# Kernel optimization log

Measured on AMD Instinct MI355X. Metric: run time of the kernel, lower is better.

Reference implementation:

```python
import jax, jax.numpy as jnp
import numpy as np

# dims: batch, samples, agents, obs_dim, action_dim, hidden
B, S, N, D, A, H = 512, 64, 8, 64, 16, 256
IN_DIM = (D + A) * N  # 640


def mish(x):
    return x * jnp.tanh(jax.nn.softplus(x))


def setup_inputs() -> dict:
    key = jax.random.key(0)
    ks = jax.random.split(key, 9)
    u = lambda k, shape, fan_in: jax.random.uniform(
        k, shape, jnp.float32, -1.0 / np.sqrt(fan_in), 1.0 / np.sqrt(fan_in))
    return {
        "state": jax.random.normal(ks[0], (B, N, D), jnp.float32),
        "action": jax.random.normal(ks[1], (B, N, A), jnp.float32),
        "W1": u(ks[2], (IN_DIM, H), IN_DIM),
        "b1": u(ks[3], (H,), IN_DIM),
        "W2": u(ks[4], (H, H), H),
        "b2": u(ks[5], (H,), H),
        "W3": u(ks[6], (H, 1), H),
        "b3": u(ks[7], (1,), H),
        # random grand-coalition permutations of the N agents, per (batch, sample)
        "perm": jnp.argsort(jax.random.uniform(ks[8], (B, S, N)), axis=-1).astype(jnp.int32),
    }


def reference(state, action, W1, b1, W2, b2, W3, b3, perm):
    # subcoalition mask [B,S,N,N]: torch builds one-hot(perm) @ tril(ones),
    # i.e. mask[b,s,i,j] = 1 iff j <= perm[b,s,i]
    subcoal = (jnp.arange(N) <= perm[..., None]).astype(state.dtype)
    # gathered actions in coalition order [B,S,N,A]: act_g[b,s,j] = action[b, perm[b,s,j]]
    act_g = action[jnp.arange(B)[:, None, None], perm]
    # masked subcoalition actions [B,S,N,N,A] -> [B,S,N,N*A]
    act = (act_g[:, :, None, :, :] * subcoal[..., None]).reshape(B, S, N, N * A)
    # flattened global obs broadcast over (sample, agent) axes [B,S,N,N*D]
    obs = jnp.broadcast_to(state.reshape(B, 1, 1, N * D), (B, S, N, N * D))
    x = jnp.concatenate([obs, act], axis=-1)  # [B,S,N,IN_DIM]
    # per-agent loop in torch uses shared q1 weights -> single batched MLP
    h = mish(x @ W1 + b1)
    h = mish(h @ W2 + b2)
    q = h @ W3 + b3                   # [B,S,N,1]
    q1 = q.mean(axis=1).squeeze(-1)   # mean over samples -> [B,N]
    return (q1, q1)
```

## Files before the change

### kernel.cpp

```cpp
#include <hip/hip_runtime.h>

typedef unsigned short ushort_t;
typedef _Float16 half_t;
typedef __attribute__((ext_vector_type(2))) _Float16 half2_t;
typedef __attribute__((ext_vector_type(8))) _Float16 half8_t;
typedef __attribute__((ext_vector_type(2))) __fp16 fp16x2;
typedef __attribute__((ext_vector_type(2))) float fx2;
typedef __attribute__((ext_vector_type(4))) float floatx4;

#define LOG2E 1.4426950408889634f
#define LN2   0.6931471805599453f

__device__ __forceinline__ float exp2_(float x) {
#if __has_builtin(__builtin_amdgcn_exp2f)
    return __builtin_amdgcn_exp2f(x);
#else
    return exp2f(x);
#endif
}

__device__ __forceinline__ half2_t cvt_pk_f16(float a, float b) {
    auto r = __builtin_amdgcn_cvt_pkrtz(a, b);
    return __builtin_bit_cast(half2_t, r);
}

__device__ __forceinline__ float fdot2_(half2_t a, half2_t b) {
#if __has_builtin(__builtin_amdgcn_fdot2)
    return __builtin_amdgcn_fdot2(__builtin_bit_cast(fp16x2, a),
                                  __builtin_bit_cast(fp16x2, b), 0.0f, false);
#else
    return (float)a.x * (float)b.x + (float)a.y * (float)b.y;
#endif
}

__device__ __forceinline__ fx2 mish2(fx2 t0) {
    fx2 one = {1.0f, 1.0f};
    fx2 m2  = {-2.0f, -2.0f};
    fx2 u   = {exp2_(t0.x), exp2_(t0.y)};
    fx2 s   = u + one;
    fx2 wv  = __builtin_elementwise_fma(s, s, one);
    fx2 rr  = {__builtin_amdgcn_rcpf(wv.x), __builtin_amdgcn_rcpf(wv.y)};
    fx2 v   = __builtin_elementwise_fma(rr, m2, one);
    return t0 * v;
}

__device__ __forceinline__ float dpp_sum16(float v) {
    int x = __float_as_int(v);
    v += __int_as_float(__builtin_amdgcn_update_dpp(0, x, 0xB1, 0xF, 0xF, true));
    x = __float_as_int(v);
    v += __int_as_float(__builtin_amdgcn_update_dpp(0, x, 0x4E, 0xF, 0xF, true));
    x = __float_as_int(v);
    v += __int_as_float(__builtin_amdgcn_update_dpp(0, x, 0x124, 0xF, 0xF, true));
    x = __float_as_int(v);
    v += __int_as_float(__builtin_amdgcn_update_dpp(0, x, 0x128, 0xF, 0xF, true));
    return v;
}

__global__ __launch_bounds__(256) void prep_kernel(
        const float* __restrict__ state,
        const float* __restrict__ action,
        const float* __restrict__ W1,
        const float* __restrict__ W2,
        float* __restrict__ obsWp,
        half_t* __restrict__ actW,
        half_t* __restrict__ W2T,
        float* __restrict__ out) {
    int bid = blockIdx.x;
    int t = threadIdx.x;
    if (bid < 512) {
        int bg = bid >> 3;
        int kc = bid & 7;
        int bs = bg * 8;
        const float* w1p = W1 + (size_t)(kc * 64) * 256 + t;
        const float* stp = state + (size_t)bs * 512 + kc * 64;
        float acc[8];
#pragma unroll
        for (int bb = 0; bb < 8; ++bb) acc[bb] = 0.f;
#pragma unroll 4
        for (int f = 0; f < 64; ++f) {
            float w = w1p[f * 256];
#pragma unroll
            for (int bb = 0; bb < 8; ++bb)
                acc[bb] = fmaf(stp[bb * 512 + f], w, acc[bb]);
        }
#pragma unroll
        for (int bb = 0; bb < 8; ++bb)
            obsWp[(size_t)kc * 131072 + (bs + bb) * 256 + t] = acc[bb];
    } else if (bid < 1536) {
        int idx = bid - 512;
        int j = idx & 7;
        int b0 = (idx >> 3) * 4;
        const float* W1a = W1 + (size_t)(512 + j * 16) * 256;
        float wv[16];
#pragma unroll
        for (int a = 0; a < 16; ++a) wv[a] = W1a[a * 256 + t];
#pragma unroll
        for (int bb = 0; bb < 4; ++bb) {
            int b = b0 + bb;
            const float* acp = action + (size_t)b * 128;
            float acc[8];
#pragma unroll
            for (int n = 0; n < 8; ++n) acc[n] = 0.f;
#pragma unroll
            for (int a = 0; a < 16; ++a) {
#pragma unroll
                for (int n = 0; n < 8; ++n)
                    acc[n] = fmaf(acp[n * 16 + a], wv[a], acc[n]);
            }
#pragma unroll
            for (int n = 0; n < 8; ++n)
                actW[(((size_t)b * 8 + n) * 8 + j) * 256 + t] = (half_t)(acc[n] * LOG2E);
        }
    } else {
        int blk = bid - 1536;
        if (blk < 16) {
            out[blk * 512 + t] = 0.0f;
            out[blk * 512 + 256 + t] = 0.0f;
        }
        int n = blk * 8 + (t >> 5);
        int klo = t & 31;
#pragma unroll
        for (int kk = 0; kk < 8; ++kk) {
            int k = kk * 32 + klo;
            W2T[n * 256 + k] = (half_t)W2[k * 256 + n];
        }
    }
}

#define CHUNK_US 528

__global__ __launch_bounds__(512, 4) void main_kernel(
        const float* __restrict__ obsWp, const half_t* __restrict__ actW,
        const half_t* __restrict__ W2T, const int* __restrict__ perm,
        const float* __restrict__ b1, const float* __restrict__ b2,
        const float* __restrict__ W3, const float* __restrict__ b3,
        float* __restrict__ out) {
    __shared__ __align__(16) ushort_t h1[2][32 * CHUNK_US];
    __shared__ __align__(16) float obsb[256];
    __shared__ int perm_s[128];
    __shared__ float qpart[2][8][64];

    int t = threadIdx.x;
    int bid = blockIdx.x;
    int b = (bid & 7) * 64 + ((bid >> 3) & 63);
    int sgp = bid >> 9;
    int s0 = sgp * 16;

    int w = t >> 6;
    int L = t & 63;
    int lo = L & 15;
    int q = L >> 4;

    const half_t* w2base = W2T + ((size_t)(w * 32 + lo)) * 256 + q * 8;
    half8_t bpre[4];
    bpre[0] = *reinterpret_cast<const half8_t*>(w2base + 0 * 4096 + 0 * 32);
    bpre[1] = *reinterpret_cast<const half8_t*>(w2base + 1 * 4096 + 0 * 32);
    bpre[2] = *reinterpret_cast<const half8_t*>(w2base + 0 * 4096 + 1 * 32);
    bpre[3] = *reinterpret_cast<const half8_t*>(w2base + 1 * 4096 + 1 * 32);

    int col0 = w * 32 + lo;
    int col1 = col0 + 16;
    fx2 b2p = {b2[col0] * LOG2E, b2[col1] * LOG2E};
    half2_t w3p = cvt_pk_f16(W3[col0] * LN2, W3[col1] * LN2);

    const int* prow = perm + ((size_t)b * 64 + s0 + w) * 8;
    int4 pa0 = *reinterpret_cast<const int4*>(prow);
    int4 pa1 = *reinterpret_cast<const int4*>(prow + 4);
    int4 pb0 = *reinterpret_cast<const int4*>(prow + 64);
    int4 pb1 = *reinterpret_cast<const int4*>(prow + 68);

    if (t < 256) {
        float s = b1[t];
#pragma unroll
        for (int c = 0; c < 8; ++c) s += obsWp[(size_t)c * 131072 + b * 256 + t];
        obsb[t] = s * LOG2E;
    } else if (t < 384) {
        perm_s[t - 256] = perm[((size_t)b * 64 + s0) * 8 + (t - 256)];
    }

    int g = L >> 1;
    int ksg = g >> 2;
    int qq = g & 3;
    int halfsel = L & 1;
    const half_t* actg = actW + (size_t)b * 64 * 256 + L * 4;
    int dstoff = qq * 128 + halfsel * 4 + ksg * CHUNK_US;

    int pj0[8] = {pa0.x, pa0.y, pa0.z, pa0.w, pa1.x, pa1.y, pa1.z, pa1.w};
    uint2 av0[8];
#pragma unroll
    for (int j = 0; j < 8; ++j)
        av0[j] = *reinterpret_cast<const uint2*>(actg + (pj0[j] * 8 + j) * 256);

    __syncthreads();

    float4 ob = *reinterpret_cast<const float4*>(obsb + L * 4);

    {
        fx2 r01 = {ob.x, ob.y};
        fx2 r23 = {ob.z, ob.w};
        ushort_t* dst0 = h1[0] + dstoff;
#pragma unroll
        for (int j = 0; j < 8; ++j) {
            half2_t a0 = __builtin_bit_cast(half2_t, av0[j].x);
            half2_t a1 = __builtin_bit_cast(half2_t, av0[j].y);
            r01 += (fx2){(float)a0.x, (float)a0.y};
            r23 += (fx2){(float)a1.x, (float)a1.y};
            fx2 h01 = mish2(r01);
            fx2 h23 = mish2(r23);
            int row = w * 8 + j;
            int mt2 = row >> 4, lr = row & 15;
            uint2 pk = make_uint2(__builtin_bit_cast(unsigned, cvt_pk_f16(h01.x, h01.y)),
                                  __builtin_bit_cast(unsigned, cvt_pk_f16(h23.x, h23.y)));
            *reinterpret_cast<uint2*>(dst0 + mt2 * 8 * CHUNK_US + lr * 8) = pk;
        }
    }

    int pj1[8] = {pb0.x, pb0.y, pb0.z, pb0.w, pb1.x, pb1.y, pb1.z, pb1.w};
    uint2 av1[8];
#pragma unroll
    for (int j = 0; j < 8; ++j)
        av1[j] = *reinterpret_cast<const uint2*>(actg + (pj1[j] * 8 + j) * 256);

    __syncthreads();

    floatx4 acc0[4][2];
#pragma unroll
    for (int mt = 0; mt < 4; ++mt)
#pragma unroll
        for (int nt = 0; nt < 2; ++nt) acc0[mt][nt] = (floatx4){0.f, 0.f, 0.f, 0.f};
    {
        fx2 r01 = {ob.x, ob.y};
        fx2 r23 = {ob.z, ob.w};
        ushort_t* dst1 = h1[1] + dstoff;
        const ushort_t* h1b0 = h1[0] + L * 8;
#pragma unroll
        for (int ks = 0; ks < 8; ++ks) {
            half8_t afr[4];
#pragma unroll
            for (int mt = 0; mt < 4; ++mt)
                afr[mt] = *reinterpret_cast<const half8_t*>(h1b0 + (mt * 8 + ks) * CHUNK_US);
            half8_t bfr0 = (ks == 0) ? bpre[0] : (ks == 1) ? bpre[2]
                         : *reinterpret_cast<const half8_t*>(w2base + 0 * 4096 + ks * 32);
            half8_t bfr1 = (ks == 0) ? bpre[1] : (ks == 1) ? bpre[3]
                         : *reinterpret_cast<const half8_t*>(w2base + 1 * 4096 + ks * 32);
#pragma unroll
            for (int mt = 0; mt < 4; ++mt) {
                acc0[mt][0] = __builtin_amdgcn_mfma_f32_16x16x32_f16(afr[mt], bfr0, acc0[mt][0], 0, 0, 0);
                acc0[mt][1] = __builtin_amdgcn_mfma_f32_16x16x32_f16(afr[mt], bfr1, acc0[mt][1], 0, 0, 0);
            }
            {
                half2_t a0 = __builtin_bit_cast(half2_t, av1[ks].x);
                half2_t a1 = __builtin_bit_cast(half2_t, av1[ks].y);
                r01 += (fx2){(float)a0.x, (float)a0.y};
                r23 += (fx2){(float)a1.x, (float)a1.y};
                fx2 h01 = mish2(r01);
                fx2 h23 = mish2(r23);
                int row = w * 8 + ks;
                int mt2 = row >> 4, lr = row & 15;
                uint2 pk = make_uint2(__builtin_bit_cast(unsigned, cvt_pk_f16(h01.x, h01.y)),
                                      __builtin_bit_cast(unsigned, cvt_pk_f16(h23.x, h23.y)));
                *reinterpret_cast<uint2*>(dst1 + mt2 * 8 * CHUNK_US + lr * 8) = pk;
            }
        }
    }
    __syncthreads();

    floatx4 acc1[4][2];
#pragma unroll
    for (int mt = 0; mt < 4; ++mt)
#pragma unroll
        for (int nt = 0; nt < 2; ++nt) acc1[mt][nt] = (floatx4){0.f, 0.f, 0.f, 0.f};
    {
        const ushort_t* h1b1 = h1[1] + L * 8;
#pragma unroll
        for (int ks = 0; ks < 8; ++ks) {
            half8_t afr[4];
#pragma unroll
            for (int mt = 0; mt < 4; ++mt)
                afr[mt] = *reinterpret_cast<const half8_t*>(h1b1 + (mt * 8 + ks) * CHUNK_US);
            half8_t bfr0 = (ks == 0) ? bpre[0] : (ks == 1) ? bpre[2]
                         : *reinterpret_cast<const half8_t*>(w2base + 0 * 4096 + ks * 32);
            half8_t bfr1 = (ks == 0) ? bpre[1] : (ks == 1) ? bpre[3]
                         : *reinterpret_cast<const half8_t*>(w2base + 1 * 4096 + ks * 32);
#pragma unroll
            for (int mt = 0; mt < 4; ++mt) {
                acc1[mt][0] = __builtin_amdgcn_mfma_f32_16x16x32_f16(afr[mt], bfr0, acc1[mt][0], 0, 0, 0);
                acc1[mt][1] = __builtin_amdgcn_mfma_f32_16x16x32_f16(afr[mt], bfr1, acc1[mt][1], 0, 0, 0);
            }
#pragma unroll
            for (int v = 0; v < 2; ++v) {
                int idx = ks * 2 + v;
                int mt = idx >> 2, r = idx & 3;
                fx2 t2 = {acc0[mt][0][r], acc0[mt][1][r]};
                t2 += b2p;
                fx2 hh = mish2(t2);
                float part = fdot2_(cvt_pk_f16(hh.x, hh.y), w3p);
                float s = dpp_sum16(part);
                if (lo == 0) qpart[0][w][mt * 16 + q * 4 + r] = s;
            }
        }
    }
#pragma unroll
    for (int idx = 0; idx < 16; ++idx) {
        int mt = idx >> 2, r = idx & 3;
        fx2 t2 = {acc1[mt][0][r], acc1[mt][1][r]};
        t2 += b2p;
        fx2 hh = mish2(t2);
        float part = fdot2_(cvt_pk_f16(hh.x, hh.y), w3p);
        float s = dpp_sum16(part);
        if (lo == 0) qpart[1][w][mt * 16 + q * 4 + r] = s;
    }
    __syncthreads();

    if (t < 16) {
        int h = t >> 3, i = t & 7;
        float p = 0.f;
#pragma unroll
        for (int sl = 0; sl < 8; ++sl) {
            int k = perm_s[(h * 8 + sl) * 8 + i];
            int row = sl * 8 + k;
            float qv = b3[0];
#pragma unroll
            for (int ww = 0; ww < 8; ++ww) qv += qpart[h][ww][row];
            p += qv;
        }
        p *= (1.0f / 64.0f);
        atomicAdd(&out[b * 8 + i], p);
        atomicAdd(&out[4096 + b * 8 + i], p);
    }
}

extern "C" void kernel_launch(void* const* d_in, const int* in_sizes, int n_in,
                              void* d_out, int out_size, void* d_ws, size_t ws_size,
                              hipStream_t stream) {
    const float* state  = (const float*)d_in[0];
    const float* action = (const float*)d_in[1];
    const float* W1     = (const float*)d_in[2];
    const float* b1     = (const float*)d_in[3];
    const float* W2     = (const float*)d_in[4];
    const float* b2     = (const float*)d_in[5];
    const float* W3     = (const float*)d_in[6];
    const float* b3     = (const float*)d_in[7];
    const int*   perm   = (const int*)d_in[8];
    float* out = (float*)d_out;

    char* ws = (char*)d_ws;
    float*  obsWp = (float*)ws;
    half_t* actW  = (half_t*)(ws + 4194304);
    half_t* W2T   = (half_t*)(ws + 4194304 + 16777216);

    prep_kernel<<<1568, 256, 0, stream>>>(state, action, W1, W2, obsWp, actW, W2T, out);
    main_kernel<<<2048, 512, 0, stream>>>(obsWp, actW, W2T, perm, b1, b2, W3, b3, out);
}
```

Before: 166.0 us.

## Process all sample groups per block in a loop, launching one block per batch

The main kernel now launches one block per batch element and loops over four sample groups, where before each group had its own block. The per-batch setup (obs bias sum, W2 prefetch, bias/W3 loads) is amortized across groups, and the next group's action gathers are issued before the barrier. This reduces the grid to 512 blocks, fewer than the 256 CUs can host at the stated occupancy, so latency hiding may suffer. An extra barrier-to-barrier dependency between iterations on the qpart buffer is also introduced.

```diff
diff --git a/kernel.cpp b/kernel.cpp
--- a/kernel.cpp
+++ b/kernel.cpp
@@ -137,14 +137,12 @@
         float* __restrict__ out) {
     __shared__ __align__(16) ushort_t h1[2][32 * CHUNK_US];
     __shared__ __align__(16) float obsb[256];
-    __shared__ int perm_s[128];
+    __shared__ int perm_s[512];
     __shared__ float qpart[2][8][64];
 
     int t = threadIdx.x;
     int bid = blockIdx.x;
     int b = (bid & 7) * 64 + ((bid >> 3) & 63);
-    int sgp = bid >> 9;
-    int s0 = sgp * 16;
 
     int w = t >> 6;
     int L = t & 63;
@@ -162,21 +160,19 @@
     int col1 = col0 + 16;
     fx2 b2p = {b2[col0] * LOG2E, b2[col1] * LOG2E};
     half2_t w3p = cvt_pk_f16(W3[col0] * LN2, W3[col1] * LN2);
-
-    const int* prow = perm + ((size_t)b * 64 + s0 + w) * 8;
+    float b3v = b3[0];
+
+    const int* prow = perm + ((size_t)b * 64 + w) * 8;
     int4 pa0 = *reinterpret_cast<const int4*>(prow);
     int4 pa1 = *reinterpret_cast<const int4*>(prow + 4);
-    int4 pb0 = *reinterpret_cast<const int4*>(prow + 64);
-    int4 pb1 = *reinterpret_cast<const int4*>(prow + 68);
 
     if (t < 256) {
         float s = b1[t];
 #pragma unroll
         for (int c = 0; c < 8; ++c) s += obsWp[(size_t)c * 131072 + b * 256 + t];
         obsb[t] = s * LOG2E;
-    } else if (t < 384) {
-        perm_s[t - 256] = perm[((size_t)b * 64 + s0) * 8 + (t - 256)];
     }
+    perm_s[t] = perm[(size_t)b * 512 + t];
 
     int g = L >> 1;
     int ksg = g >> 2;
@@ -195,138 +191,151 @@
 
     float4 ob = *reinterpret_cast<const float4*>(obsb + L * 4);
 
-    {
-        fx2 r01 = {ob.x, ob.y};
-        fx2 r23 = {ob.z, ob.w};
-        ushort_t* dst0 = h1[0] + dstoff;
-#pragma unroll
-        for (int j = 0; j < 8; ++j) {
-            half2_t a0 = __builtin_bit_cast(half2_t, av0[j].x);
-            half2_t a1 = __builtin_bit_cast(half2_t, av0[j].y);
-            r01 += (fx2){(float)a0.x, (float)a0.y};
-            r23 += (fx2){(float)a1.x, (float)a1.y};
-            fx2 h01 = mish2(r01);
-            fx2 h23 = mish2(r23);
-            int row = w * 8 + j;
-            int mt2 = row >> 4, lr = row & 15;
-            uint2 pk = make_uint2(__builtin_bit_cast(unsigned, cvt_pk_f16(h01.x, h01.y)),
-                                  __builtin_bit_cast(unsigned, cvt_pk_f16(h23.x, h23.y)));
-            *reinterpret_cast<uint2*>(dst0 + mt2 * 8 * CHUNK_US + lr * 8) = pk;
-        }
-    }
-
-    int pj1[8] = {pb0.x, pb0.y, pb0.z, pb0.w, pb1.x, pb1.y, pb1.z, pb1.w};
     uint2 av1[8];
-#pragma unroll
-    for (int j = 0; j < 8; ++j)
-        av1[j] = *reinterpret_cast<const uint2*>(actg + (pj1[j] * 8 + j) * 256);
-
-    __syncthreads();
-
-    floatx4 acc0[4][2];
-#pragma unroll
-    for (int mt = 0; mt < 4; ++mt)
-#pragma unroll
-        for (int nt = 0; nt < 2; ++nt) acc0[mt][nt] = (floatx4){0.f, 0.f, 0.f, 0.f};
-    {
-        fx2 r01 = {ob.x, ob.y};
-        fx2 r23 = {ob.z, ob.w};
-        ushort_t* dst1 = h1[1] + dstoff;
-        const ushort_t* h1b0 = h1[0] + L * 8;
-#pragma unroll
-        for (int ks = 0; ks < 8; ++ks) {
-            half8_t afr[4];
-#pragma unroll
-            for (int mt = 0; mt < 4; ++mt)
-                afr[mt] = *reinterpret_cast<const half8_t*>(h1b0 + (mt * 8 + ks) * CHUNK_US);
-            half8_t bfr0 = (ks == 0) ? bpre[0] : (ks == 1) ? bpre[2]
-                         : *reinterpret_cast<const half8_t*>(w2base + 0 * 4096 + ks * 32);
-            half8_t bfr1 = (ks == 0) ? bpre[1] : (ks == 1) ? bpre[3]
-                         : *reinterpret_cast<const half8_t*>(w2base + 1 * 4096 + ks * 32);
-#pragma unroll
-            for (int mt = 0; mt < 4; ++mt) {
-                acc0[mt][0] = __builtin_amdgcn_mfma_f32_16x16x32_f16(afr[mt], bfr0, acc0[mt][0], 0, 0, 0);
-                acc0[mt][1] = __builtin_amdgcn_mfma_f32_16x16x32_f16(afr[mt], bfr1, acc0[mt][1], 0, 0, 0);
-            }
-            {
-                half2_t a0 = __builtin_bit_cast(half2_t, av1[ks].x);
-                half2_t a1 = __builtin_bit_cast(half2_t, av1[ks].y);
+    floatx4 acc0[4][2], acc1[4][2];
+
+#pragma unroll 1
+    for (int sg = 0; sg < 4; ++sg) {
+        {
+            fx2 r01 = {ob.x, ob.y};
+            fx2 r23 = {ob.z, ob.w};
+            ushort_t* dst0 = h1[0] + dstoff;
+#pragma unroll
+            for (int j = 0; j < 8; ++j) {
+                half2_t a0 = __builtin_bit_cast(half2_t, av0[j].x);
+                half2_t a1 = __builtin_bit_cast(half2_t, av0[j].y);
                 r01 += (fx2){(float)a0.x, (float)a0.y};
                 r23 += (fx2){(float)a1.x, (float)a1.y};
                 fx2 h01 = mish2(r01);
                 fx2 h23 = mish2(r23);
-                int row = w * 8 + ks;
+                int row = w * 8 + j;
                 int mt2 = row >> 4, lr = row & 15;
                 uint2 pk = make_uint2(__builtin_bit_cast(unsigned, cvt_pk_f16(h01.x, h01.y)),
                                       __builtin_bit_cast(unsigned, cvt_pk_f16(h23.x, h23.y)));
-                *reinterpret_cast<uint2*>(dst1 + mt2 * 8 * CHUNK_US + lr * 8) = pk;
-            }
-        }
-    }
-    __syncthreads();
-
-    floatx4 acc1[4][2];
-#pragma unroll
-    for (int mt = 0; mt < 4; ++mt)
-#pragma unroll
-        for (int nt = 0; nt < 2; ++nt) acc1[mt][nt] = (floatx4){0.f, 0.f, 0.f, 0.f};
-    {
-        const ushort_t* h1b1 = h1[1] + L * 8;
-#pragma unroll
-        for (int ks = 0; ks < 8; ++ks) {
-            half8_t afr[4];
-#pragma unroll
-            for (int mt = 0; mt < 4; ++mt)
-                afr[mt] = *reinterpret_cast<const half8_t*>(h1b1 + (mt * 8 + ks) * CHUNK_US);
-            half8_t bfr0 = (ks == 0) ? bpre[0] : (ks == 1) ? bpre[2]
-                         : *reinterpret_cast<const half8_t*>(w2base + 0 * 4096 + ks * 32);
-            half8_t bfr1 = (ks == 0) ? bpre[1] : (ks == 1) ? bpre[3]
-                         : *reinterpret_cast<const half8_t*>(w2base + 1 * 4096 + ks * 32);
-#pragma unroll
-            for (int mt = 0; mt < 4; ++mt) {
-                acc1[mt][0] = __builtin_amdgcn_mfma_f32_16x16x32_f16(afr[mt], bfr0, acc1[mt][0], 0, 0, 0);
-                acc1[mt][1] = __builtin_amdgcn_mfma_f32_16x16x32_f16(afr[mt], bfr1, acc1[mt][1], 0, 0, 0);
-            }
-#pragma unroll
-            for (int v = 0; v < 2; ++v) {
-                int idx = ks * 2 + v;
-                int mt = idx >> 2, r = idx & 3;
-                fx2 t2 = {acc0[mt][0][r], acc0[mt][1][r]};
-                t2 += b2p;
-                fx2 hh = mish2(t2);
-                float part = fdot2_(cvt_pk_f16(hh.x, hh.y), w3p);
-                float s = dpp_sum16(part);
-                if (lo == 0) qpart[0][w][mt * 16 + q * 4 + r] = s;
-            }
-        }
-    }
-#pragma unroll
-    for (int idx = 0; idx < 16; ++idx) {
-        int mt = idx >> 2, r = idx & 3;
-        fx2 t2 = {acc1[mt][0][r], acc1[mt][1][r]};
-        t2 += b2p;
-        fx2 hh = mish2(t2);
-        float part = fdot2_(cvt_pk_f16(hh.x, hh.y), w3p);
-        float s = dpp_sum16(part);
-        if (lo == 0) qpart[1][w][mt * 16 + q * 4 + r] = s;
-    }
-    __syncthreads();
-
-    if (t < 16) {
-        int h = t >> 3, i = t & 7;
-        float p = 0.f;
-#pragma unroll
-        for (int sl = 0; sl < 8; ++sl) {
-            int k = perm_s[(h * 8 + sl) * 8 + i];
-            int row = sl * 8 + k;
-            float qv = b3[0];
-#pragma unroll
-            for (int ww = 0; ww < 8; ++ww) qv += qpart[h][ww][row];
-            p += qv;
-        }
-        p *= (1.0f / 64.0f);
-        atomicAdd(&out[b * 8 + i], p);
-        atomicAdd(&out[4096 + b * 8 + i], p);
+                *reinterpret_cast<uint2*>(dst0 + mt2 * 8 * CHUNK_US + lr * 8) = pk;
+            }
+        }
+
+#pragma unroll
+        for (int j = 0; j < 8; ++j) {
+            int p = perm_s[(sg * 16 + 8 + w) * 8 + j];
+            av1[j] = *reinterpret_cast<const uint2*>(actg + (p * 8 + j) * 256);
+        }
+
+        __syncthreads();
+
+#pragma unroll
+        for (int mt = 0; mt < 4; ++mt)
+#pragma unroll
+            for (int nt = 0; nt < 2; ++nt) acc0[mt][nt] = (floatx4){0.f, 0.f, 0.f, 0.f};
+        {
+            fx2 r01 = {ob.x, ob.y};
+            fx2 r23 = {ob.z, ob.w};
+            ushort_t* dst1 = h1[1] + dstoff;
+            const ushort_t* h1b0 = h1[0] + L * 8;
+#pragma unroll
+            for (int ks = 0; ks < 8; ++ks) {
+                half8_t afr[4];
+#pragma unroll
+                for (int mt = 0; mt < 4; ++mt)
+                    afr[mt] = *reinterpret_cast<const half8_t*>(h1b0 + (mt * 8 + ks) * CHUNK_US);
+                half8_t bfr0 = (ks == 0) ? bpre[0] : (ks == 1) ? bpre[2]
+                             : *reinterpret_cast<const half8_t*>(w2base + 0 * 4096 + ks * 32);
+                half8_t bfr1 = (ks == 0) ? bpre[1] : (ks == 1) ? bpre[3]
+                             : *reinterpret_cast<const half8_t*>(w2base + 1 * 4096 + ks * 32);
+#pragma unroll
+                for (int mt = 0; mt < 4; ++mt) {
+                    acc0[mt][0] = __builtin_amdgcn_mfma_f32_16x16x32_f16(afr[mt], bfr0, acc0[mt][0], 0, 0, 0);
+                    acc0[mt][1] = __builtin_amdgcn_mfma_f32_16x16x32_f16(afr[mt], bfr1, acc0[mt][1], 0, 0, 0);
+                }
+                {
+                    half2_t a0 = __builtin_bit_cast(half2_t, av1[ks].x);
+                    half2_t a1 = __builtin_bit_cast(half2_t, av1[ks].y);
+                    r01 += (fx2){(float)a0.x, (float)a0.y};
+                    r23 += (fx2){(float)a1.x, (float)a1.y};
+                    fx2 h01 = mish2(r01);
+                    fx2 h23 = mish2(r23);
+                    int row = w * 8 + ks;
+                    int mt2 = row >> 4, lr = row & 15;
+                    uint2 pk = make_uint2(__builtin_bit_cast(unsigned, cvt_pk_f16(h01.x, h01.y)),
+                                          __builtin_bit_cast(unsigned, cvt_pk_f16(h23.x, h23.y)));
+                    *reinterpret_cast<uint2*>(dst1 + mt2 * 8 * CHUNK_US + lr * 8) = pk;
+                }
+            }
+        }
+        __syncthreads();
+
+#pragma unroll
+        for (int mt = 0; mt < 4; ++mt)
+#pragma unroll
+            for (int nt = 0; nt < 2; ++nt) acc1[mt][nt] = (floatx4){0.f, 0.f, 0.f, 0.f};
+        {
+            const ushort_t* h1b1 = h1[1] + L * 8;
+#pragma unroll
+            for (int ks = 0; ks < 8; ++ks) {
+                half8_t afr[4];
+#pragma unroll
+                for (int mt = 0; mt < 4; ++mt)
+                    afr[mt] = *reinterpret_cast<const half8_t*>(h1b1 + (mt * 8 + ks) * CHUNK_US);
+                half8_t bfr0 = (ks == 0) ? bpre[0] : (ks == 1) ? bpre[2]
+                             : *reinterpret_cast<const half8_t*>(w2base + 0 * 4096 + ks * 32);
+                half8_t bfr1 = (ks == 0) ? bpre[1] : (ks == 1) ? bpre[3]
+                             : *reinterpret_cast<const half8_t*>(w2base + 1 * 4096 + ks * 32);
+#pragma unroll
+                for (int mt = 0; mt < 4; ++mt) {
+                    acc1[mt][0] = __builtin_amdgcn_mfma_f32_16x16x32_f16(afr[mt], bfr0, acc1[mt][0], 0, 0, 0);
+                    acc1[mt][1] = __builtin_amdgcn_mfma_f32_16x16x32_f16(afr[mt], bfr1, acc1[mt][1], 0, 0, 0);
+                }
+#pragma unroll
+                for (int v = 0; v < 2; ++v) {
+                    int idx = ks * 2 + v;
+                    int mt = idx >> 2, r = idx & 3;
+                    fx2 t2 = {acc0[mt][0][r], acc0[mt][1][r]};
+                    t2 += b2p;
+                    fx2 hh = mish2(t2);
+                    float part = fdot2_(cvt_pk_f16(hh.x, hh.y), w3p);
+                    float s = dpp_sum16(part);
+                    if (lo == 0) qpart[0][w][mt * 16 + q * 4 + r] = s;
+                }
+            }
+        }
+#pragma unroll
+        for (int idx = 0; idx < 16; ++idx) {
+            int mt = idx >> 2, r = idx & 3;
+            fx2 t2 = {acc1[mt][0][r], acc1[mt][1][r]};
+            t2 += b2p;
+            fx2 hh = mish2(t2);
+            float part = fdot2_(cvt_pk_f16(hh.x, hh.y), w3p);
+            float s = dpp_sum16(part);
+            if (lo == 0) qpart[1][w][mt * 16 + q * 4 + r] = s;
+        }
+
+        if (sg < 3) {
+#pragma unroll
+            for (int j = 0; j < 8; ++j) {
+                int p = perm_s[((sg + 1) * 16 + w) * 8 + j];
+                av0[j] = *reinterpret_cast<const uint2*>(actg + (p * 8 + j) * 256);
+            }
+        }
+
+        __syncthreads();
+
+        if (t < 16) {
+            int h = t >> 3, i = t & 7;
+            float p = 0.f;
+#pragma unroll
+            for (int sl = 0; sl < 8; ++sl) {
+                int k = perm_s[(sg * 16 + h * 8 + sl) * 8 + i];
+                int row = sl * 8 + k;
+                float qv = b3v;
+#pragma unroll
+                for (int ww = 0; ww < 8; ++ww) qv += qpart[h][ww][row];
+                p += qv;
+            }
+            p *= (1.0f / 64.0f);
+            atomicAdd(&out[b * 8 + i], p);
+            atomicAdd(&out[4096 + b * 8 + i], p);
+        }
     }
 }
 
@@ -350,5 +359,5 @@
     half_t* W2T   = (half_t*)(ws + 4194304 + 16777216);
 
     prep_kernel<<<1568, 256, 0, stream>>>(state, action, W1, W2, obsWp, actW, W2T, out);
-    main_kernel<<<2048, 512, 0, stream>>>(obsWp, actW, W2T, perm, b1, b2, W3, b3, out);
-}
+    main_kernel<<<512, 512, 0, stream>>>(obsWp, actW, W2T, perm, b1, b2, W3, b3, out);
+}
```

Measured after the change: 180.8 us. +8.9%, slower.
